# Kernel optimization log

Hardware: AMD Instinct MI355X
Metric: run time of the kernel (lower is better)

Reference implementation:

```python
import jax, jax.numpy as jnp
import numpy as np

HIDDEN_DIM = 512
RADIUS = 128


def rel_pos_indexes(seq_len_q: int, seq_len_k: int, radius: int):
    # (i - j) clamped to [-radius, radius], shifted to [0, 2*radius]
    i = jnp.arange(seq_len_k)[None, :]   # [1, Sk]
    j = jnp.arange(seq_len_q)[:, None]   # [Sq, 1]
    return jnp.clip(i - j, -radius, radius) + radius  # [Sq, Sk] int


def setup_inputs() -> dict:
    key = jax.random.key(0)
    kq, kk, kv, ke = jax.random.split(key, 4)
    B, Sq, Sk, d = 4, 2048, 2048, HIDDEN_DIM
    Q = jax.random.normal(kq, (B, Sq, d), dtype=jnp.float32)
    K = jax.random.normal(kk, (B, Sk, d), dtype=jnp.float32)
    V = jax.random.normal(kv, (B, Sk, d), dtype=jnp.float32)
    # learned relative-position embedding table: (2R+1, d)
    rel_embeds = jax.random.normal(ke, (2 * RADIUS + 1, d), dtype=jnp.float32)
    return {"Q": Q, "K": K, "V": V, "rel_embeds": rel_embeds}


def reference(Q, K, V, rel_embeds):
    B, Sq, d = Q.shape
    Sk = K.shape[1]
    normalizer = jnp.asarray(d ** 0.5, dtype=Q.dtype)
    # content scores: [B, Sq, Sk]
    energy = jnp.einsum('bqd,bkd->bqk', Q, K)
    # relative scores: Q against the (2R+1) relative embeddings -> [B, Sq, 2R+1]
    Q_rel = jnp.einsum('bqd,rd->bqr', Q, rel_embeds)
    idx = rel_pos_indexes(Sq, Sk, RADIUS)  # [Sq, Sk]
    # gather along last dim per query row (same index map for every batch)
    rel_shift = jnp.take_along_axis(Q_rel, idx[None, :, :].repeat(B, axis=0), axis=2)
    energy = (energy + rel_shift) / normalizer
    attn = jax.nn.softmax(energy, axis=2)
    Z = jnp.einsum('bqk,bkd->bqd', attn, V)
    return attn, Z
```

## Files before the change

kernel.cpp:

```cpp
#include <hip/hip_runtime.h>

#define BATCH 4
#define SQL 2048
#define SKL 2048
#define DIM 512
#define NR 257
#define NRP 288
#define RAD 128

typedef __bf16 bf16x8 __attribute__((ext_vector_type(8)));
typedef float f32x4 __attribute__((ext_vector_type(4)));
typedef unsigned short u16;
typedef u16 u16x4 __attribute__((ext_vector_type(4)));
typedef u16 u16x8 __attribute__((ext_vector_type(8)));

__device__ inline u16 f2bf(float x) {
  union { float f; unsigned u; } v; v.f = x;
  unsigned r = v.u + 0x7FFF + ((v.u >> 16) & 1);
  return (u16)(r >> 16);
}

__device__ inline void glds16(const u16* g, const u16* l) {
  __builtin_amdgcn_global_load_lds(
      (const __attribute__((address_space(1))) void*)g,
      (__attribute__((address_space(3))) void*)l, 16, 0, 0);
}


__global__ void cvt_kernel(const f32x4* __restrict__ src, u16x4* __restrict__ dst, int n4) {
  int i = blockIdx.x * 256 + threadIdx.x;
  if (i >= n4) return;
  f32x4 f = src[i];
  u16x4 o;
#pragma unroll
  for (int e = 0; e < 4; e++) o[e] = f2bf(f[e]);
  dst[i] = o;
}

__global__ void cvt_rel_kernel(const float* __restrict__ rel, u16* __restrict__ relb) {
  int i = blockIdx.x * 256 + threadIdx.x;
  int r = i >> 9;
  relb[i] = (r < NR) ? f2bf(rel[i]) : (u16)0;
}

__global__ void transpose_v_kernel(const float* __restrict__ V, u16* __restrict__ Vt) {
  __shared__ float tile[32][33];
  int b = blockIdx.z;
  int k0 = blockIdx.x * 32, d0 = blockIdx.y * 32;
  int tx = threadIdx.x, ty = threadIdx.y;
#pragma unroll
  for (int r = 0; r < 4; r++)
    tile[ty + r * 8][tx] = V[((long)b * SKL + k0 + ty + r * 8) * DIM + d0 + tx];
  __syncthreads();
#pragma unroll
  for (int r = 0; r < 4; r++)
    Vt[((long)b * DIM + d0 + ty + r * 8) * SKL + k0 + tx] = f2bf(tile[tx][ty + r * 8]);
}

__global__ __launch_bounds__(256) void qrel_kernel(const u16* __restrict__ Qb,
                                                   const u16* __restrict__ relb,
                                                   float* __restrict__ Qrel) {
  int tid = threadIdx.x;
  int wave = tid >> 6, lane = tid & 63;
  int m0 = blockIdx.x * 64 + wave * 16;
  int j0 = blockIdx.y * 2;
  int fr = lane & 15, fk = (lane >> 4) * 8;
  f32x4 acc[2] = {};
  const u16* qrow = Qb + (long)(m0 + fr) * DIM + fk;
  const u16* r0 = relb + (long)(j0 * 16 + fr) * DIM + fk;
  const u16* r1 = r0 + 16 * DIM;
  for (int k0 = 0; k0 < DIM; k0 += 32) {
    bf16x8 a = *(const bf16x8*)(qrow + k0);
    bf16x8 b0 = *(const bf16x8*)(r0 + k0);
    bf16x8 b1 = *(const bf16x8*)(r1 + k0);
    acc[0] = __builtin_amdgcn_mfma_f32_16x16x32_bf16(a, b0, acc[0], 0, 0, 0);
    acc[1] = __builtin_amdgcn_mfma_f32_16x16x32_bf16(a, b1, acc[1], 0, 0, 0);
  }
  int cr = (lane >> 4) * 4, cc = lane & 15;
#pragma unroll
  for (int t = 0; t < 2; t++)
#pragma unroll
    for (int r = 0; r < 4; r++)
      Qrel[(long)(m0 + cr + r) * NRP + (j0 + t) * 16 + cc] = acc[t][r];
}

__global__ __launch_bounds__(256) void energy_kernel(const u16* __restrict__ Qb,
                                                     const u16* __restrict__ Kb,
                                                     const float* __restrict__ Qrel,
                                                     u16* __restrict__ S) {
  int b = blockIdx.z;
  int m0 = blockIdx.y * 128;
  int n0 = blockIdx.x * 128;
  const u16* A = Qb + (long)b * SQL * DIM;
  const u16* Bp = Kb + (long)b * SKL * DIM;
  __shared__ u16 As[128 * 32];
  __shared__ u16 Bs[128 * 32];
  int tid = threadIdx.x;
  int wave = tid >> 6, lane = tid & 63;
  int wm = (wave >> 1) * 64, wn = (wave & 1) * 64;
  int fr = lane & 15, fk = (lane >> 4) * 8;
  int srow = wave * 32 + (lane >> 2);
  int scol = (lane & 3) * 8;
  f32x4 acc[4][4] = {};
  for (int k0 = 0; k0 < DIM; k0 += 32) {
    __syncthreads();
    glds16(A + (long)(m0 + srow) * DIM + k0 + scol, As + (wave * 2 + 0) * 512);
    glds16(A + (long)(m0 + srow + 16) * DIM + k0 + scol, As + (wave * 2 + 1) * 512);
    glds16(Bp + (long)(n0 + srow) * DIM + k0 + scol, Bs + (wave * 2 + 0) * 512);
    glds16(Bp + (long)(n0 + srow + 16) * DIM + k0 + scol, Bs + (wave * 2 + 1) * 512);
    __syncthreads();
    bf16x8 af[4], bfr[4];
#pragma unroll
    for (int i = 0; i < 4; i++) af[i] = *(const bf16x8*)(As + (wm + i * 16 + fr) * 32 + fk);
#pragma unroll
    for (int j = 0; j < 4; j++) bfr[j] = *(const bf16x8*)(Bs + (wn + j * 16 + fr) * 32 + fk);
#pragma unroll
    for (int i = 0; i < 4; i++)
#pragma unroll
      for (int j = 0; j < 4; j++)
        acc[i][j] = __builtin_amdgcn_mfma_f32_16x16x32_bf16(af[i], bfr[j], acc[i][j], 0, 0, 0);
  }
  const float inv_norm = 0.04419417382415922f;
  int cr = (lane >> 4) * 4, cc = lane & 15;
#pragma unroll
  for (int i = 0; i < 4; i++) {
#pragma unroll
    for (int r = 0; r < 4; r++) {
      int q = m0 + wm + i * 16 + cr + r;
      const float* qrow = Qrel + ((long)b * SQL + q) * NRP;
      u16* sr = S + ((long)b * SQL + q) * SKL;
#pragma unroll
      for (int j = 0; j < 4; j++) {
        int k = n0 + wn + j * 16 + cc;
        int dlt = k - q;
        dlt = dlt < -RAD ? -RAD : (dlt > RAD ? RAD : dlt);
        sr[k] = f2bf((acc[i][j][r] + qrow[dlt + RAD]) * inv_norm);
      }
    }
  }
}

__global__ __launch_bounds__(256) void softmax_kernel(u16* __restrict__ S,
                                                      float* __restrict__ attn) {
  long row = blockIdx.x;
  u16* srow = S + row * SKL;
  float* arow = attn + row * SKL;
  int tid = threadIdx.x;
  int wave = tid >> 6, lane = tid & 63;
  bf16x8 v = *(const bf16x8*)(srow + tid * 8);
  float f[8];
#pragma unroll
  for (int e = 0; e < 8; e++) f[e] = (float)v[e];
  float m = -1e30f;
#pragma unroll
  for (int e = 0; e < 8; e++) m = fmaxf(m, f[e]);
  for (int o = 32; o > 0; o >>= 1) m = fmaxf(m, __shfl_xor(m, o));
  __shared__ float red[4];
  if (lane == 0) red[wave] = m;
  __syncthreads();
  m = fmaxf(fmaxf(red[0], red[1]), fmaxf(red[2], red[3]));
  __syncthreads();
  float s = 0.0f;
  float e8[8];
#pragma unroll
  for (int e = 0; e < 8; e++) { e8[e] = __expf(f[e] - m); s += e8[e]; }
  for (int o = 32; o > 0; o >>= 1) s += __shfl_xor(s, o);
  if (lane == 0) red[wave] = s;
  __syncthreads();
  s = red[0] + red[1] + red[2] + red[3];
  float inv = 1.0f / s;
  f32x4 o0, o1;
  u16x8 pb;
#pragma unroll
  for (int e = 0; e < 4; e++) {
    float p = e8[e] * inv;
    o0[e] = p; pb[e] = f2bf(p);
  }
#pragma unroll
  for (int e = 0; e < 4; e++) {
    float p = e8[e + 4] * inv;
    o1[e] = p; pb[e + 4] = f2bf(p);
  }
  *(f32x4*)(arow + tid * 8) = o0;
  *(f32x4*)(arow + tid * 8 + 4) = o1;
  *(u16x8*)(srow + tid * 8) = pb;
}

__global__ __launch_bounds__(256) void z_kernel(const u16* __restrict__ S,
                                                const u16* __restrict__ Vt,
                                                float* __restrict__ Z) {
  int b = blockIdx.z;
  int m0 = blockIdx.y * 64;
  int n0 = blockIdx.x * 128;
  const u16* A = S + (long)b * SQL * SKL;
  const u16* Bp = Vt + (long)b * DIM * SKL;
  __shared__ u16 As[64 * 32];
  __shared__ u16 Bs[128 * 32];
  int tid = threadIdx.x;
  int wave = tid >> 6, lane = tid & 63;
  int wm = (wave >> 1) * 32, wn = (wave & 1) * 64;
  int fr = lane & 15, fk = (lane >> 4) * 8;
  int srowA = wave * 16 + (lane >> 2);
  int srowB = wave * 32 + (lane >> 2);
  int scol = (lane & 3) * 8;
  f32x4 acc[2][4] = {};
  for (int k0 = 0; k0 < SKL; k0 += 32) {
    __syncthreads();
    glds16(A + (long)(m0 + srowA) * SKL + k0 + scol, As + wave * 512);
    glds16(Bp + (long)(n0 + srowB) * SKL + k0 + scol, Bs + (wave * 2 + 0) * 512);
    glds16(Bp + (long)(n0 + srowB + 16) * SKL + k0 + scol, Bs + (wave * 2 + 1) * 512);
    __syncthreads();
    bf16x8 af[2], bfr[4];
#pragma unroll
    for (int i = 0; i < 2; i++) af[i] = *(const bf16x8*)(As + (wm + i * 16 + fr) * 32 + fk);
#pragma unroll
    for (int j = 0; j < 4; j++) bfr[j] = *(const bf16x8*)(Bs + (wn + j * 16 + fr) * 32 + fk);
#pragma unroll
    for (int i = 0; i < 2; i++)
#pragma unroll
      for (int j = 0; j < 4; j++)
        acc[i][j] = __builtin_amdgcn_mfma_f32_16x16x32_bf16(af[i], bfr[j], acc[i][j], 0, 0, 0);
  }
  int cr = (lane >> 4) * 4, cc = lane & 15;
#pragma unroll
  for (int i = 0; i < 2; i++)
#pragma unroll
    for (int r = 0; r < 4; r++) {
      int q = m0 + wm + i * 16 + cr + r;
      float* zrow = Z + ((long)b * SQL + q) * DIM;
#pragma unroll
      for (int j = 0; j < 4; j++)
        zrow[n0 + wn + j * 16 + cc] = acc[i][j][r];
    }
}


extern "C" void kernel_launch(void* const* d_in, const int* in_sizes, int n_in,
                              void* d_out, int out_size, void* d_ws, size_t ws_size,
                              hipStream_t stream) {
  const float* Q = (const float*)d_in[0];
  const float* K = (const float*)d_in[1];
  const float* V = (const float*)d_in[2];
  const float* rel = (const float*)d_in[3];
  float* attn = (float*)d_out;
  float* Z = attn + (long)BATCH * SQL * SKL;

  char* ws = (char*)d_ws;
  u16* Qb   = (u16*)ws;
  u16* Kb   = (u16*)(ws + 8388608);
  u16* Vt   = (u16*)(ws + 16777216);
  u16* relb = (u16*)(ws + 25165824);
  float* Qrel = (float*)(ws + 25460736);
  u16* S    = (u16*)(ws + 34897920);

  cvt_kernel<<<4096, 256, 0, stream>>>((const f32x4*)Q, (u16x4*)Qb, 1048576);
  cvt_kernel<<<4096, 256, 0, stream>>>((const f32x4*)K, (u16x4*)Kb, 1048576);
  cvt_rel_kernel<<<576, 256, 0, stream>>>(rel, relb);
  transpose_v_kernel<<<dim3(64, 16, BATCH), dim3(32, 8), 0, stream>>>(V, Vt);
  qrel_kernel<<<dim3(128, 9), 256, 0, stream>>>(Qb, relb, Qrel);
  energy_kernel<<<dim3(16, 16, BATCH), 256, 0, stream>>>(Qb, Kb, Qrel, S);
  softmax_kernel<<<8192, 256, 0, stream>>>(S, attn);
  z_kernel<<<dim3(4, 32, BATCH), 256, 0, stream>>>(S, Vt, Z);
}
```

Baseline: 248.6 us.

## Double K-step to 64 in energy and Z GEMMs, reshape Z tiles, merge cvt launches

The energy and Z GEMM kernels now stage a 64-wide K slice per iteration instead of 32, which halves the number of barrier pairs and issues two MFMA k-substeps per tile load. The Z kernel moves from 64x128 to 32x256 output tiles, so each wave covers all 32 rows and a 64-column strip, changing how A and B tiles are reused. The two Q/K conversion launches are merged into one 2D grid. The cost is more LDS per block, which may lower occupancy, and the Z tile has a lower A:B reuse balance.

```diff
diff --git a/kernel.cpp b/kernel.cpp
--- a/kernel.cpp
+++ b/kernel.cpp
@@ -27,9 +27,11 @@
 }
 
 
-__global__ void cvt_kernel(const f32x4* __restrict__ src, u16x4* __restrict__ dst, int n4) {
+__global__ void cvt_qk_kernel(const f32x4* __restrict__ Q, const f32x4* __restrict__ K,
+                              u16x4* __restrict__ Qb, u16x4* __restrict__ Kb) {
   int i = blockIdx.x * 256 + threadIdx.x;
-  if (i >= n4) return;
+  const f32x4* src = blockIdx.y ? K : Q;
+  u16x4* dst = blockIdx.y ? Kb : Qb;
   f32x4 f = src[i];
   u16x4 o;
 #pragma unroll
@@ -93,32 +95,39 @@
   int n0 = blockIdx.x * 128;
   const u16* A = Qb + (long)b * SQL * DIM;
   const u16* Bp = Kb + (long)b * SKL * DIM;
-  __shared__ u16 As[128 * 32];
-  __shared__ u16 Bs[128 * 32];
+  __shared__ u16 As[128 * 64];
+  __shared__ u16 Bs[128 * 64];
   int tid = threadIdx.x;
   int wave = tid >> 6, lane = tid & 63;
   int wm = (wave >> 1) * 64, wn = (wave & 1) * 64;
   int fr = lane & 15, fk = (lane >> 4) * 8;
-  int srow = wave * 32 + (lane >> 2);
-  int scol = (lane & 3) * 8;
+  int sr8 = lane >> 3;
+  int sc = (lane & 7) * 8;
   f32x4 acc[4][4] = {};
-  for (int k0 = 0; k0 < DIM; k0 += 32) {
-    __syncthreads();
-    glds16(A + (long)(m0 + srow) * DIM + k0 + scol, As + (wave * 2 + 0) * 512);
-    glds16(A + (long)(m0 + srow + 16) * DIM + k0 + scol, As + (wave * 2 + 1) * 512);
-    glds16(Bp + (long)(n0 + srow) * DIM + k0 + scol, Bs + (wave * 2 + 0) * 512);
-    glds16(Bp + (long)(n0 + srow + 16) * DIM + k0 + scol, Bs + (wave * 2 + 1) * 512);
-    __syncthreads();
-    bf16x8 af[4], bfr[4];
-#pragma unroll
-    for (int i = 0; i < 4; i++) af[i] = *(const bf16x8*)(As + (wm + i * 16 + fr) * 32 + fk);
-#pragma unroll
-    for (int j = 0; j < 4; j++) bfr[j] = *(const bf16x8*)(Bs + (wn + j * 16 + fr) * 32 + fk);
-#pragma unroll
-    for (int i = 0; i < 4; i++)
-#pragma unroll
-      for (int j = 0; j < 4; j++)
-        acc[i][j] = __builtin_amdgcn_mfma_f32_16x16x32_bf16(af[i], bfr[j], acc[i][j], 0, 0, 0);
+  for (int k0 = 0; k0 < DIM; k0 += 64) {
+    __syncthreads();
+#pragma unroll
+    for (int t = 0; t < 4; t++) {
+      int issue = wave * 4 + t;
+      glds16(A + (long)(m0 + issue * 8 + sr8) * DIM + k0 + sc, As + issue * 512);
+      glds16(Bp + (long)(n0 + issue * 8 + sr8) * DIM + k0 + sc, Bs + issue * 512);
+    }
+    __syncthreads();
+    bf16x8 af[2][4], bfr[2][4];
+#pragma unroll
+    for (int t = 0; t < 2; t++) {
+#pragma unroll
+      for (int i = 0; i < 4; i++) af[t][i] = *(const bf16x8*)(As + (wm + i * 16 + fr) * 64 + t * 32 + fk);
+#pragma unroll
+      for (int j = 0; j < 4; j++) bfr[t][j] = *(const bf16x8*)(Bs + (wn + j * 16 + fr) * 64 + t * 32 + fk);
+    }
+#pragma unroll
+    for (int t = 0; t < 2; t++)
+#pragma unroll
+      for (int i = 0; i < 4; i++)
+#pragma unroll
+        for (int j = 0; j < 4; j++)
+          acc[i][j] = __builtin_amdgcn_mfma_f32_16x16x32_bf16(af[t][i], bfr[t][j], acc[i][j], 0, 0, 0);
   }
   const float inv_norm = 0.04419417382415922f;
   int cr = (lane >> 4) * 4, cc = lane & 15;
@@ -190,43 +199,50 @@
                                                 const u16* __restrict__ Vt,
                                                 float* __restrict__ Z) {
   int b = blockIdx.z;
-  int m0 = blockIdx.y * 64;
-  int n0 = blockIdx.x * 128;
+  int m0 = blockIdx.y * 32;
+  int n0 = blockIdx.x * 256;
   const u16* A = S + (long)b * SQL * SKL;
   const u16* Bp = Vt + (long)b * DIM * SKL;
-  __shared__ u16 As[64 * 32];
-  __shared__ u16 Bs[128 * 32];
-  int tid = threadIdx.x;
-  int wave = tid >> 6, lane = tid & 63;
-  int wm = (wave >> 1) * 32, wn = (wave & 1) * 64;
+  __shared__ u16 As[32 * 64];
+  __shared__ u16 Bs[256 * 64];
+  int tid = threadIdx.x;
+  int wave = tid >> 6, lane = tid & 63;
+  int wn = wave * 64;
   int fr = lane & 15, fk = (lane >> 4) * 8;
-  int srowA = wave * 16 + (lane >> 2);
-  int srowB = wave * 32 + (lane >> 2);
-  int scol = (lane & 3) * 8;
+  int sr8 = lane >> 3;
+  int sc = (lane & 7) * 8;
   f32x4 acc[2][4] = {};
-  for (int k0 = 0; k0 < SKL; k0 += 32) {
-    __syncthreads();
-    glds16(A + (long)(m0 + srowA) * SKL + k0 + scol, As + wave * 512);
-    glds16(Bp + (long)(n0 + srowB) * SKL + k0 + scol, Bs + (wave * 2 + 0) * 512);
-    glds16(Bp + (long)(n0 + srowB + 16) * SKL + k0 + scol, Bs + (wave * 2 + 1) * 512);
-    __syncthreads();
-    bf16x8 af[2], bfr[4];
-#pragma unroll
-    for (int i = 0; i < 2; i++) af[i] = *(const bf16x8*)(As + (wm + i * 16 + fr) * 32 + fk);
-#pragma unroll
-    for (int j = 0; j < 4; j++) bfr[j] = *(const bf16x8*)(Bs + (wn + j * 16 + fr) * 32 + fk);
-#pragma unroll
-    for (int i = 0; i < 2; i++)
-#pragma unroll
-      for (int j = 0; j < 4; j++)
-        acc[i][j] = __builtin_amdgcn_mfma_f32_16x16x32_bf16(af[i], bfr[j], acc[i][j], 0, 0, 0);
+  for (int k0 = 0; k0 < SKL; k0 += 64) {
+    __syncthreads();
+    glds16(A + (long)(m0 + wave * 8 + sr8) * SKL + k0 + sc, As + wave * 512);
+#pragma unroll
+    for (int t = 0; t < 8; t++) {
+      int issue = wave * 8 + t;
+      glds16(Bp + (long)(n0 + issue * 8 + sr8) * SKL + k0 + sc, Bs + issue * 512);
+    }
+    __syncthreads();
+    bf16x8 af[2][2], bfr[2][4];
+#pragma unroll
+    for (int t = 0; t < 2; t++) {
+#pragma unroll
+      for (int i = 0; i < 2; i++) af[t][i] = *(const bf16x8*)(As + (i * 16 + fr) * 64 + t * 32 + fk);
+#pragma unroll
+      for (int j = 0; j < 4; j++) bfr[t][j] = *(const bf16x8*)(Bs + (wn + j * 16 + fr) * 64 + t * 32 + fk);
+    }
+#pragma unroll
+    for (int t = 0; t < 2; t++)
+#pragma unroll
+      for (int i = 0; i < 2; i++)
+#pragma unroll
+        for (int j = 0; j < 4; j++)
+          acc[i][j] = __builtin_amdgcn_mfma_f32_16x16x32_bf16(af[t][i], bfr[t][j], acc[i][j], 0, 0, 0);
   }
   int cr = (lane >> 4) * 4, cc = lane & 15;
 #pragma unroll
   for (int i = 0; i < 2; i++)
 #pragma unroll
     for (int r = 0; r < 4; r++) {
-      int q = m0 + wm + i * 16 + cr + r;
+      int q = m0 + i * 16 + cr + r;
       float* zrow = Z + ((long)b * SQL + q) * DIM;
 #pragma unroll
       for (int j = 0; j < 4; j++)
@@ -253,12 +269,12 @@
   float* Qrel = (float*)(ws + 25460736);
   u16* S    = (u16*)(ws + 34897920);
 
-  cvt_kernel<<<4096, 256, 0, stream>>>((const f32x4*)Q, (u16x4*)Qb, 1048576);
-  cvt_kernel<<<4096, 256, 0, stream>>>((const f32x4*)K, (u16x4*)Kb, 1048576);
+  cvt_qk_kernel<<<dim3(4096, 2), 256, 0, stream>>>((const f32x4*)Q, (const f32x4*)K,
+                                                   (u16x4*)Qb, (u16x4*)Kb);
   cvt_rel_kernel<<<576, 256, 0, stream>>>(rel, relb);
   transpose_v_kernel<<<dim3(64, 16, BATCH), dim3(32, 8), 0, stream>>>(V, Vt);
   qrel_kernel<<<dim3(128, 9), 256, 0, stream>>>(Qb, relb, Qrel);
   energy_kernel<<<dim3(16, 16, BATCH), 256, 0, stream>>>(Qb, Kb, Qrel, S);
   softmax_kernel<<<8192, 256, 0, stream>>>(S, attn);
-  z_kernel<<<dim3(4, 32, BATCH), 256, 0, stream>>>(S, Vt, Z);
-}
+  z_kernel<<<dim3(2, 64, BATCH), 256, 0, stream>>>(S, Vt, Z);
+}
```

Result: slower. 264.6 us (+6.4%).
